# Optimization experiments

Measured on AMD Instinct MI355X. Metric: run time of the kernel, lower is better.

Reference implementation:

```python
import jax, jax.numpy as jnp
import numpy as np

B, L, C, H = 4, 2048, 768, 12
D = C // H
MAX_SCALE_MUL = float(np.log(100.0))
BLOCK = 128  # block size for the VAR-style block-causal mask


def _block_causal_bias(L, block):
    # 0 where key-block <= query-block, -inf elsewhere (block lower-triangular)
    bid = np.arange(L) // block
    vis = bid[:, None] >= bid[None, :]
    bias = np.where(vis, 0.0, -np.inf).astype(np.float32)
    return jnp.asarray(bias)[None, None]  # (1,1,L,L)


def setup_inputs() -> dict:
    key = jax.random.key(0)
    ks = jax.random.split(key, 5)
    x = jax.random.normal(ks[0], (B, L, C), dtype=jnp.float32)
    W_qkv = jax.random.normal(ks[1], (3 * C, C), dtype=jnp.float32) * (1.0 / np.sqrt(C))
    q_bias = jnp.zeros((C,), jnp.float32)
    v_bias = jnp.zeros((C,), jnp.float32)
    # module inits scale_mul to log(4.0)
    log_scale_mul = jnp.full((1, H, 1, 1), np.log(4.0), jnp.float32)
    W_proj = jax.random.normal(ks[2], (C, C), dtype=jnp.float32) * (1.0 / np.sqrt(C))
    b_proj = jnp.zeros((C,), jnp.float32)
    attn_bias = _block_causal_bias(L, BLOCK)
    return {"x": x, "attn_bias": attn_bias, "W_qkv": W_qkv, "q_bias": q_bias,
            "v_bias": v_bias, "log_scale_mul": log_scale_mul,
            "W_proj": W_proj, "b_proj": b_proj}


def _l2norm(t, eps=1e-12):
    n = jnp.linalg.norm(t, axis=-1, keepdims=True)
    return t / jnp.maximum(n, eps)


def reference(x, attn_bias, W_qkv, q_bias, v_bias, log_scale_mul, W_proj, b_proj):
    Bx, Lx, Cx = x.shape
    # qkv projection with concatenated (q_bias, zero_k_bias, v_bias)
    bias = jnp.concatenate([q_bias, jnp.zeros_like(q_bias), v_bias])
    qkv = x @ W_qkv.T + bias                      # (B,L,3C)
    qkv = qkv.reshape(Bx, Lx, 3, H, D)
    q, k, v = jnp.moveaxis(qkv, 2, 0)             # each (B,L,H,D)
    q = jnp.swapaxes(q, 1, 2)                     # (B,H,L,D)
    k = jnp.swapaxes(k, 1, 2)
    v = jnp.swapaxes(v, 1, 2)
    # cos-attention: L2-normalize q,k; head-wise learnable scale on q; scale=1
    scale_mul = jnp.exp(jnp.minimum(log_scale_mul, MAX_SCALE_MUL))  # (1,H,1,1)
    q = _l2norm(q) * scale_mul
    k = _l2norm(k)
    scores = jnp.einsum('bhld,bhmd->bhlm', q, k) + attn_bias
    attn = jax.nn.softmax(scores, axis=-1)
    o = jnp.einsum('bhlm,bhmd->bhld', attn, v)    # (B,H,L,D)
    o = jnp.swapaxes(o, 1, 2).reshape(Bx, Lx, Cx)
    return o @ W_proj.T + b_proj
```

## Files before the change

### kernel.cpp

```cpp
#include <hip/hip_runtime.h>
#include <hip/hip_bf16.h>

#define DEV __device__ __forceinline__

typedef __bf16 bf16x8 __attribute__((ext_vector_type(8)));
typedef float  f32x4  __attribute__((ext_vector_type(4)));

typedef __attribute__((address_space(3))) unsigned int LDSU;
typedef __attribute__((address_space(1))) const unsigned int GLBU;

DEV unsigned short f2b(float f){
  __bf16 h = (__bf16)f;
  return __builtin_bit_cast(unsigned short, h);
}

static constexpr float MAXLOG = 4.60517018598809136804f;
static constexpr float L2E    = 1.44269504088896340736f;

DEV ushort4 cvt4(float4 v){
  ushort4 o; o.x = f2b(v.x); o.y = f2b(v.y); o.z = f2b(v.z); o.w = f2b(v.w); return o;
}
__global__ void cvt3_kernel(const float4* __restrict__ a, ushort4* __restrict__ da, int na,
                            const float4* __restrict__ b, ushort4* __restrict__ db, int nb,
                            const float4* __restrict__ c, ushort4* __restrict__ dc, int nc){
  int i = blockIdx.x * 256 + threadIdx.x;
  if (i < na) { da[i] = cvt4(a[i]); return; }
  i -= na;
  if (i < nb) { db[i] = cvt4(b[i]); return; }
  i -= nb;
  if (i < nc) { dc[i] = cvt4(c[i]); }
}

__global__ __launch_bounds__(512) void qkv_gemm(
    const unsigned short* __restrict__ X,
    const unsigned short* __restrict__ W,
    const float* __restrict__ qbias, const float* __restrict__ vbias,
    const float* __restrict__ lsm,
    unsigned short* __restrict__ Qo, unsigned short* __restrict__ Ko,
    unsigned short* __restrict__ Vo)
{
  __shared__ char smem[65536];
  const int tid = threadIdx.x;
  const int l = tid & 63, w = tid >> 6;
  const int wr = w >> 1, wc = w & 1;
  const int lr = l & 15, lg = l >> 4;
  const int tm = blockIdx.x % 64;
  const int tn = blockIdx.x / 64;
  const int m0 = tm * 128, n0 = tn * 128;

  f32x4 acc[2][4];
  #pragma unroll
  for (int i=0;i<2;i++)
    #pragma unroll
    for (int j=0;j<4;j++) acc[i][j] = (f32x4){0.f,0.f,0.f,0.f};

  #pragma unroll
  for (int c=0;c<2;++c){
    int chunk = c*512 + tid;
    int row = chunk >> 3;
    int scc = (chunk & 7) ^ (row & 7);
    __builtin_amdgcn_global_load_lds((GLBU*)(X + (size_t)(m0+row)*768 + scc*8),
                                     (LDSU*)(smem + chunk*16), 16, 0, 0);
    __builtin_amdgcn_global_load_lds((GLBU*)(W + (size_t)(n0+row)*768 + scc*8),
                                     (LDSU*)(smem + 32768 + chunk*16), 16, 0, 0);
  }

  for (int kt = 0; kt < 12; ++kt){
    __syncthreads();
    const int pc = kt & 1;
    char* Acur = smem + pc*16384;
    char* Bcur = smem + 32768 + pc*16384;

    if (kt + 1 < 12){
      const int k1 = (kt+1)*64;
      char* Anxt = smem + (pc^1)*16384;
      char* Bnxt = smem + 32768 + (pc^1)*16384;
      #pragma unroll
      for (int c=0;c<2;++c){
        int chunk = c*512 + tid;
        int row = chunk >> 3;
        int scc = (chunk & 7) ^ (row & 7);
        __builtin_amdgcn_global_load_lds((GLBU*)(X + (size_t)(m0+row)*768 + k1 + scc*8),
                                         (LDSU*)(Anxt + chunk*16), 16, 0, 0);
        __builtin_amdgcn_global_load_lds((GLBU*)(W + (size_t)(n0+row)*768 + k1 + scc*8),
                                         (LDSU*)(Bnxt + chunk*16), 16, 0, 0);
      }
    }

    #pragma unroll
    for (int kk = 0; kk < 2; ++kk){
      bf16x8 af[2], bfv[4];
      #pragma unroll
      for (int m=0;m<2;m++){
        int row = wr*32 + m*16 + lr;
        int byte = kk*64 + lg*16;
        af[m] = *(const bf16x8*)(Acur + row*128 + (byte ^ ((row&7)<<4)));
      }
      #pragma unroll
      for (int n=0;n<4;n++){
        int row = wc*64 + n*16 + lr;
        int byte = kk*64 + lg*16;
        bfv[n] = *(const bf16x8*)(Bcur + row*128 + (byte ^ ((row&7)<<4)));
      }
      #pragma unroll
      for (int m=0;m<2;m++)
        #pragma unroll
        for (int n=0;n<4;n++)
          acc[m][n] = __builtin_amdgcn_mfma_f32_16x16x32_bf16(af[m], bfv[n], acc[m][n], 0, 0, 0);
    }
  }

  const int nb = n0 + wc*64;
  const int seg = nb / 768;
  const int h = (nb % 768) / 64;
  float mul = 1.0f;
  if (seg == 0) mul = __expf(fminf(lsm[h], MAXLOG)) * L2E;
  float bias_v[4];
  #pragma unroll
  for (int n=0;n<4;n++){
    int d = n*16 + lr;
    bias_v[n] = (seg==0) ? qbias[h*64+d] : (seg==2 ? vbias[h*64+d] : 0.f);
  }
  unsigned short* dst = (seg==0) ? Qo : (seg==1 ? Ko : Vo);
  #pragma unroll
  for (int m=0;m<2;m++){
    #pragma unroll
    for (int r=0;r<4;r++){
      float vals[4]; float ss = 0.f;
      #pragma unroll
      for (int n=0;n<4;n++){ float v = acc[m][n][r] + bias_v[n]; vals[n] = v; ss += v*v; }
      ss += __shfl_xor(ss,1); ss += __shfl_xor(ss,2);
      ss += __shfl_xor(ss,4); ss += __shfl_xor(ss,8);
      float sc = (seg==2) ? 1.f : mul / fmaxf(sqrtf(ss), 1e-12f);
      int grow = m0 + wr*32 + m*16 + lg*4 + r;
      int b = grow >> 11, lrow = grow & 2047;
      size_t base = (((size_t)(b*12 + h))*2048 + lrow)*64;
      #pragma unroll
      for (int n=0;n<4;n++) dst[base + n*16 + lr] = f2b(vals[n]*sc);
    }
  }
}

__global__ __launch_bounds__(512) void attn_kernel(
    const unsigned short* __restrict__ Q,
    const unsigned short* __restrict__ K,
    const unsigned short* __restrict__ V,
    const float* __restrict__ lsm,
    unsigned short* __restrict__ O)
{
  __shared__ char smem[49152];
  const int tid = threadIdx.x;
  const int l = tid & 63, w = tid >> 6;
  char* Plds = smem + 32768 + w*2048;
  const int lr = l & 15, lg = l >> 4;

  const int bid = blockIdx.x;
  const int qb = 15 - (bid / 48);
  const int bh = bid % 48;
  const int h = bh % 12;
  const size_t plane = (size_t)bh * (2048*64);
  const int q0 = qb*128 + w*16;

  const float M = __expf(fminf(lsm[h], MAXLOG)) * L2E;

  bf16x8 qf[2];
  #pragma unroll
  for (int ki=0;ki<2;ki++)
    qf[ki] = *(const bf16x8*)(Q + plane + (size_t)(q0 + lr)*64 + ki*32 + lg*8);

  float lsum = 0.f;
  f32x4 of[4];
  #pragma unroll
  for (int di=0;di<4;di++) of[di] = (f32x4){0.f,0.f,0.f,0.f};

  const int krow = tid >> 3;
  const int kscc = (tid & 7) ^ (krow & 7);
  const int rv  = tid & 63;
  const int c0v = (tid >> 6) * 8;

  const int nt = (qb + 1) * 2;

  {
    const unsigned short* Kt0 = K + plane;
    const unsigned short* Vt0 = V + plane;
    __builtin_amdgcn_global_load_lds((GLBU*)(Kt0 + krow*64 + kscc*8),
                                     (LDSU*)(smem + tid*16), 16, 0, 0);
    bf16x8 a = *(const bf16x8*)(Vt0 + rv*64 + c0v);
    #pragma unroll
    for (int j=0;j<8;j++)
      *(__bf16*)(smem + 16384 + (c0v+j)*128 + ((2*rv) ^ (j<<4))) = a[j];
  }

  for (int t = 0; t < nt; ++t){
    __syncthreads();
    const int pc = t & 1;
    char* Kcur = smem + pc*8192;
    char* Vcur = smem + 16384 + pc*8192;
    char* Knxt = smem + (pc^1)*8192;
    char* Vnxt = smem + 16384 + (pc^1)*8192;
    const bool pre = (t+1) < nt;

    bf16x8 nv;
    if (pre){
      const unsigned short* Kt1 = K + plane + (size_t)(t+1)*4096;
      const unsigned short* Vt1 = V + plane + (size_t)(t+1)*4096;
      __builtin_amdgcn_global_load_lds((GLBU*)(Kt1 + krow*64 + kscc*8),
                                       (LDSU*)(Knxt + tid*16), 16, 0, 0);
      nv = *(const bf16x8*)(Vt1 + rv*64 + c0v);
    }

    f32x4 s[4];
    #pragma unroll
    for (int ni=0;ni<4;ni++) s[ni] = (f32x4){0.f,0.f,0.f,0.f};
    #pragma unroll
    for (int ki=0;ki<2;ki++){
      bf16x8 kb[4];
      #pragma unroll
      for (int ni=0;ni<4;ni++){
        int key = ni*16 + lr;
        int byte = ki*64 + lg*16;
        kb[ni] = *(const bf16x8*)(Kcur + key*128 + (byte ^ ((key&7)<<4)));
      }
      __builtin_amdgcn_s_setprio(1);
      #pragma unroll
      for (int ni=0;ni<4;ni++)
        s[ni] = __builtin_amdgcn_mfma_f32_16x16x32_bf16(kb[ni], qf[ki], s[ni], 0, 0, 0);
      __builtin_amdgcn_s_setprio(0);
    }

    {
      const int row = lr;
      float a16 = 0.f;
      #pragma unroll
      for (int ni=0;ni<4;ni++){
        float p0 = __builtin_amdgcn_exp2f(s[ni][0] - M);
        float p1 = __builtin_amdgcn_exp2f(s[ni][1] - M);
        float p2 = __builtin_amdgcn_exp2f(s[ni][2] - M);
        float p3 = __builtin_amdgcn_exp2f(s[ni][3] - M);
        a16 += (p0 + p1) + (p2 + p3);
        uint2 uv;
        uv.x = (unsigned)f2b(p0) | ((unsigned)f2b(p1) << 16);
        uv.y = (unsigned)f2b(p2) | ((unsigned)f2b(p3) << 16);
        *(uint2*)(Plds + row*128 + ((ni*32 + lg*8) ^ ((row&7)<<4))) = uv;
      }
      lsum += a16;
    }
    asm volatile("s_waitcnt lgkmcnt(0)" ::: "memory");
    __builtin_amdgcn_sched_barrier(0);

    #pragma unroll
    for (int ki=0;ki<2;ki++){
      bf16x8 pa, vbf[4];
      {
        int row = lr;
        int byte = ki*64 + lg*16;
        pa = *(const bf16x8*)(Plds + row*128 + (byte ^ ((row&7)<<4)));
      }
      #pragma unroll
      for (int di=0;di<4;di++){
        int d = di*16 + lr;
        int byte = ki*64 + lg*16;
        vbf[di] = *(const bf16x8*)(Vcur + d*128 + (byte ^ ((d&7)<<4)));
      }
      __builtin_amdgcn_s_setprio(1);
      #pragma unroll
      for (int di=0;di<4;di++)
        of[di] = __builtin_amdgcn_mfma_f32_16x16x32_bf16(pa, vbf[di], of[di], 0, 0, 0);
      __builtin_amdgcn_s_setprio(0);
    }

    if (pre){
      #pragma unroll
      for (int j=0;j<8;j++)
        *(__bf16*)(Vnxt + (c0v+j)*128 + ((2*rv) ^ (j<<4))) = nv[j];
    }
  }

  {
    float sum = lsum;
    sum += __shfl_xor(sum,16); sum += __shfl_xor(sum,32);
    lsum = sum;
  }
  const int b = bh / 12;
  #pragma unroll
  for (int r=0;r<4;r++){
    float inv = 1.f / __shfl(lsum, lg*4 + r);
    int row = q0 + lg*4 + r;
    size_t base = ((size_t)(b*2048) + row)*768 + h*64;
    #pragma unroll
    for (int di=0;di<4;di++)
      O[base + di*16 + lr] = f2b(of[di][r]*inv);
  }
}

__global__ __launch_bounds__(256) void proj_gemm(
    const unsigned short* __restrict__ A,
    const unsigned short* __restrict__ W,
    const float* __restrict__ bias,
    float* __restrict__ out)
{
  __shared__ char smem[16384];
  char* Alds = smem;
  char* Blds = smem + 8192;

  const int tid = threadIdx.x;
  const int l = tid & 63, w = tid >> 6;
  const int lr = l & 15, lg = l >> 4;
  const int tm = blockIdx.x % 128;
  const int tn = blockIdx.x / 128;
  const int m0 = tm * 64, n0 = tn * 64;

  f32x4 acc[4];
  #pragma unroll
  for (int j=0;j<4;j++) acc[j] = (f32x4){0.f,0.f,0.f,0.f};

  for (int kt = 0; kt < 12; ++kt){
    const int k0 = kt * 64;
    __syncthreads();
    #pragma unroll
    for (int c = 0; c < 2; ++c){
      int chunk = c*256 + tid;
      int row = chunk >> 3;
      int scc = (chunk & 7) ^ (row & 7);
      __builtin_amdgcn_global_load_lds((GLBU*)(A + (size_t)(m0+row)*768 + k0 + scc*8),
                                       (LDSU*)(Alds + (c*256 + w*64)*16), 16, 0, 0);
      __builtin_amdgcn_global_load_lds((GLBU*)(W + (size_t)(n0+row)*768 + k0 + scc*8),
                                       (LDSU*)(Blds + (c*256 + w*64)*16), 16, 0, 0);
    }
    __syncthreads();
    #pragma unroll
    for (int kk = 0; kk < 2; ++kk){
      bf16x8 af, bfv[4];
      {
        int row = w*16 + lr;
        int byte = kk*64 + lg*16;
        af = *(const bf16x8*)(Alds + row*128 + (byte ^ ((row&7)<<4)));
      }
      #pragma unroll
      for (int n=0;n<4;n++){
        int row = n*16 + lr;
        int byte = kk*64 + lg*16;
        bfv[n] = *(const bf16x8*)(Blds + row*128 + (byte ^ ((row&7)<<4)));
      }
      #pragma unroll
      for (int n=0;n<4;n++)
        acc[n] = __builtin_amdgcn_mfma_f32_16x16x32_bf16(af, bfv[n], acc[n], 0, 0, 0);
    }
  }

  #pragma unroll
  for (int r=0;r<4;r++){
    int grow = m0 + w*16 + lg*4 + r;
    #pragma unroll
    for (int n=0;n<4;n++){
      int colg = n0 + n*16 + lr;
      out[(size_t)grow*768 + colg] = acc[n][r] + bias[colg];
    }
  }
}

extern "C" void kernel_launch(void* const* d_in, const int* in_sizes, int n_in,
                              void* d_out, int out_size, void* d_ws, size_t ws_size,
                              hipStream_t stream)
{
  const float* x     = (const float*)d_in[0];
  const float* Wqkv  = (const float*)d_in[2];
  const float* qbias = (const float*)d_in[3];
  const float* vbias = (const float*)d_in[4];
  const float* lsm   = (const float*)d_in[5];
  const float* Wproj = (const float*)d_in[6];
  const float* bproj = (const float*)d_in[7];
  float* out = (float*)d_out;

  char* ws = (char*)d_ws;
  size_t off = 0;
  auto alloc = [&](size_t bytes)->char*{
    char* p = ws + off; off += (bytes + 255) & ~(size_t)255; return p;
  };
  unsigned short* xb  = (unsigned short*)alloc((size_t)8192*768*2);
  unsigned short* wqb = (unsigned short*)alloc((size_t)2304*768*2);
  unsigned short* wpb = (unsigned short*)alloc((size_t)768*768*2);
  unsigned short* qn  = (unsigned short*)alloc((size_t)48*2048*64*2);
  unsigned short* kn  = (unsigned short*)alloc((size_t)48*2048*64*2);
  unsigned short* vn  = (unsigned short*)alloc((size_t)48*2048*64*2);
  unsigned short* ob  = (unsigned short*)alloc((size_t)8192*768*2);

  cvt3_kernel<<<8448, 256, 0, stream>>>((const float4*)x,     (ushort4*)xb,  1572864,
                                        (const float4*)Wqkv,  (ushort4*)wqb,  442368,
                                        (const float4*)Wproj, (ushort4*)wpb,  147456);
  qkv_gemm<<<64*18, 512, 0, stream>>>(xb, wqb, qbias, vbias, lsm, qn, kn, vn);
  attn_kernel<<<768, 512, 0, stream>>>(qn, kn, vn, lsm, ob);
  proj_gemm<<<128*12, 256, 0, stream>>>(ob, wpb, bproj, out);
}
```

Baseline: 119.6 us.

## Double attention query tile per block to reuse K/V tiles across 256 queries

Each attention block now handles 256 query rows (32 per wave) instead of 128, so every K/V tile staged in LDS feeds twice as many MFMAs, and the grid is halved to 384 blocks. Waves in the lower half of the block skip the final key tiles that fall outside their causal range but still take part in the loads and barriers. This cuts repeated K/V global traffic and loop overhead at the cost of more LDS (64KB), more registers, fewer blocks for the 256 CUs, and some idle waves in the last tiles.

```diff
diff --git a/kernel.cpp b/kernel.cpp
--- a/kernel.cpp
+++ b/kernel.cpp
@@ -148,37 +148,42 @@
     const float* __restrict__ lsm,
     unsigned short* __restrict__ O)
 {
-  __shared__ char smem[49152];
+  __shared__ char smem[65536];
   const int tid = threadIdx.x;
   const int l = tid & 63, w = tid >> 6;
-  char* Plds = smem + 32768 + w*2048;
+  char* Plds = smem + 32768 + w*4096;
   const int lr = l & 15, lg = l >> 4;
 
   const int bid = blockIdx.x;
-  const int qb = 15 - (bid / 48);
+  const int pb = 7 - (bid / 48);
   const int bh = bid % 48;
   const int h = bh % 12;
   const size_t plane = (size_t)bh * (2048*64);
-  const int q0 = qb*128 + w*16;
+  const int q0 = pb*256 + w*32;
+
+  const int my_nt  = (2*pb + 1 + (w >> 2)) * 2;
+  const int nt_max = (2*pb + 2) * 2;
 
   const float M = __expf(fminf(lsm[h], MAXLOG)) * L2E;
 
-  bf16x8 qf[2];
-  #pragma unroll
-  for (int ki=0;ki<2;ki++)
-    qf[ki] = *(const bf16x8*)(Q + plane + (size_t)(q0 + lr)*64 + ki*32 + lg*8);
-
-  float lsum = 0.f;
-  f32x4 of[4];
-  #pragma unroll
-  for (int di=0;di<4;di++) of[di] = (f32x4){0.f,0.f,0.f,0.f};
+  bf16x8 qf[2][2];
+  #pragma unroll
+  for (int mi=0;mi<2;mi++)
+    #pragma unroll
+    for (int ki=0;ki<2;ki++)
+      qf[mi][ki] = *(const bf16x8*)(Q + plane + (size_t)(q0 + mi*16 + lr)*64 + ki*32 + lg*8);
+
+  float lsum[2] = {0.f, 0.f};
+  f32x4 of[2][4];
+  #pragma unroll
+  for (int mi=0;mi<2;mi++)
+    #pragma unroll
+    for (int di=0;di<4;di++) of[mi][di] = (f32x4){0.f,0.f,0.f,0.f};
 
   const int krow = tid >> 3;
   const int kscc = (tid & 7) ^ (krow & 7);
   const int rv  = tid & 63;
   const int c0v = (tid >> 6) * 8;
-
-  const int nt = (qb + 1) * 2;
 
   {
     const unsigned short* Kt0 = K + plane;
@@ -191,14 +196,14 @@
       *(__bf16*)(smem + 16384 + (c0v+j)*128 + ((2*rv) ^ (j<<4))) = a[j];
   }
 
-  for (int t = 0; t < nt; ++t){
+  for (int t = 0; t < nt_max; ++t){
     __syncthreads();
     const int pc = t & 1;
     char* Kcur = smem + pc*8192;
     char* Vcur = smem + 16384 + pc*8192;
     char* Knxt = smem + (pc^1)*8192;
     char* Vnxt = smem + 16384 + (pc^1)*8192;
-    const bool pre = (t+1) < nt;
+    const bool pre = (t+1) < nt_max;
 
     bf16x8 nv;
     if (pre){
@@ -209,64 +214,74 @@
       nv = *(const bf16x8*)(Vt1 + rv*64 + c0v);
     }
 
-    f32x4 s[4];
-    #pragma unroll
-    for (int ni=0;ni<4;ni++) s[ni] = (f32x4){0.f,0.f,0.f,0.f};
-    #pragma unroll
-    for (int ki=0;ki<2;ki++){
-      bf16x8 kb[4];
-      #pragma unroll
-      for (int ni=0;ni<4;ni++){
-        int key = ni*16 + lr;
-        int byte = ki*64 + lg*16;
-        kb[ni] = *(const bf16x8*)(Kcur + key*128 + (byte ^ ((key&7)<<4)));
-      }
-      __builtin_amdgcn_s_setprio(1);
-      #pragma unroll
-      for (int ni=0;ni<4;ni++)
-        s[ni] = __builtin_amdgcn_mfma_f32_16x16x32_bf16(kb[ni], qf[ki], s[ni], 0, 0, 0);
-      __builtin_amdgcn_s_setprio(0);
-    }
-
-    {
-      const int row = lr;
-      float a16 = 0.f;
-      #pragma unroll
-      for (int ni=0;ni<4;ni++){
-        float p0 = __builtin_amdgcn_exp2f(s[ni][0] - M);
-        float p1 = __builtin_amdgcn_exp2f(s[ni][1] - M);
-        float p2 = __builtin_amdgcn_exp2f(s[ni][2] - M);
-        float p3 = __builtin_amdgcn_exp2f(s[ni][3] - M);
-        a16 += (p0 + p1) + (p2 + p3);
-        uint2 uv;
-        uv.x = (unsigned)f2b(p0) | ((unsigned)f2b(p1) << 16);
-        uv.y = (unsigned)f2b(p2) | ((unsigned)f2b(p3) << 16);
-        *(uint2*)(Plds + row*128 + ((ni*32 + lg*8) ^ ((row&7)<<4))) = uv;
-      }
-      lsum += a16;
-    }
-    asm volatile("s_waitcnt lgkmcnt(0)" ::: "memory");
-    __builtin_amdgcn_sched_barrier(0);
-
-    #pragma unroll
-    for (int ki=0;ki<2;ki++){
-      bf16x8 pa, vbf[4];
-      {
-        int row = lr;
-        int byte = ki*64 + lg*16;
-        pa = *(const bf16x8*)(Plds + row*128 + (byte ^ ((row&7)<<4)));
-      }
-      #pragma unroll
-      for (int di=0;di<4;di++){
-        int d = di*16 + lr;
-        int byte = ki*64 + lg*16;
-        vbf[di] = *(const bf16x8*)(Vcur + d*128 + (byte ^ ((d&7)<<4)));
-      }
-      __builtin_amdgcn_s_setprio(1);
-      #pragma unroll
-      for (int di=0;di<4;di++)
-        of[di] = __builtin_amdgcn_mfma_f32_16x16x32_bf16(pa, vbf[di], of[di], 0, 0, 0);
-      __builtin_amdgcn_s_setprio(0);
+    if (t < my_nt){
+      f32x4 s[2][4];
+      #pragma unroll
+      for (int mi=0;mi<2;mi++)
+        #pragma unroll
+        for (int ni=0;ni<4;ni++) s[mi][ni] = (f32x4){0.f,0.f,0.f,0.f};
+      #pragma unroll
+      for (int ki=0;ki<2;ki++){
+        bf16x8 kb[4];
+        #pragma unroll
+        for (int ni=0;ni<4;ni++){
+          int key = ni*16 + lr;
+          int byte = ki*64 + lg*16;
+          kb[ni] = *(const bf16x8*)(Kcur + key*128 + (byte ^ ((key&7)<<4)));
+        }
+        __builtin_amdgcn_s_setprio(1);
+        #pragma unroll
+        for (int mi=0;mi<2;mi++)
+          #pragma unroll
+          for (int ni=0;ni<4;ni++)
+            s[mi][ni] = __builtin_amdgcn_mfma_f32_16x16x32_bf16(kb[ni], qf[mi][ki], s[mi][ni], 0, 0, 0);
+        __builtin_amdgcn_s_setprio(0);
+      }
+
+      #pragma unroll
+      for (int mi=0;mi<2;mi++){
+        const int row = mi*16 + lr;
+        float a16 = 0.f;
+        #pragma unroll
+        for (int ni=0;ni<4;ni++){
+          float p0 = __builtin_amdgcn_exp2f(s[mi][ni][0] - M);
+          float p1 = __builtin_amdgcn_exp2f(s[mi][ni][1] - M);
+          float p2 = __builtin_amdgcn_exp2f(s[mi][ni][2] - M);
+          float p3 = __builtin_amdgcn_exp2f(s[mi][ni][3] - M);
+          a16 += (p0 + p1) + (p2 + p3);
+          uint2 uv;
+          uv.x = (unsigned)f2b(p0) | ((unsigned)f2b(p1) << 16);
+          uv.y = (unsigned)f2b(p2) | ((unsigned)f2b(p3) << 16);
+          *(uint2*)(Plds + row*128 + ((ni*32 + lg*8) ^ ((row&7)<<4))) = uv;
+        }
+        lsum[mi] += a16;
+      }
+      asm volatile("s_waitcnt lgkmcnt(0)" ::: "memory");
+      __builtin_amdgcn_sched_barrier(0);
+
+      #pragma unroll
+      for (int ki=0;ki<2;ki++){
+        bf16x8 pa[2], vbf[4];
+        #pragma unroll
+        for (int mi=0;mi<2;mi++){
+          int row = mi*16 + lr;
+          int byte = ki*64 + lg*16;
+          pa[mi] = *(const bf16x8*)(Plds + row*128 + (byte ^ ((row&7)<<4)));
+        }
+        #pragma unroll
+        for (int di=0;di<4;di++){
+          int d = di*16 + lr;
+          int byte = ki*64 + lg*16;
+          vbf[di] = *(const bf16x8*)(Vcur + d*128 + (byte ^ ((d&7)<<4)));
+        }
+        __builtin_amdgcn_s_setprio(1);
+        #pragma unroll
+        for (int mi=0;mi<2;mi++)
+          #pragma unroll
+          for (int di=0;di<4;di++)
+            of[mi][di] = __builtin_amdgcn_mfma_f32_16x16x32_bf16(pa[mi], vbf[di], of[mi][di], 0, 0, 0);
+        __builtin_amdgcn_s_setprio(0);
+      }
     }
 
     if (pre){
@@ -276,20 +291,24 @@
     }
   }
 
-  {
-    float sum = lsum;
+  #pragma unroll
+  for (int mi=0;mi<2;mi++){
+    float sum = lsum[mi];
     sum += __shfl_xor(sum,16); sum += __shfl_xor(sum,32);
-    lsum = sum;
+    lsum[mi] = sum;
   }
   const int b = bh / 12;
   #pragma unroll
-  for (int r=0;r<4;r++){
-    float inv = 1.f / __shfl(lsum, lg*4 + r);
-    int row = q0 + lg*4 + r;
-    size_t base = ((size_t)(b*2048) + row)*768 + h*64;
-    #pragma unroll
-    for (int di=0;di<4;di++)
-      O[base + di*16 + lr] = f2b(of[di][r]*inv);
+  for (int mi=0;mi<2;mi++){
+    #pragma unroll
+    for (int r=0;r<4;r++){
+      float inv = 1.f / __shfl(lsum[mi], lg*4 + r);
+      int row = q0 + mi*16 + lg*4 + r;
+      size_t base = ((size_t)(b*2048) + row)*768 + h*64;
+      #pragma unroll
+      for (int di=0;di<4;di++)
+        O[base + di*16 + lr] = f2b(of[mi][di][r]*inv);
+    }
   }
 }
 
@@ -389,6 +408,6 @@
                                         (const float4*)Wqkv,  (ushort4*)wqb,  442368,
                                         (const float4*)Wproj, (ushort4*)wpb,  147456);
   qkv_gemm<<<64*18, 512, 0, stream>>>(xb, wqb, qbias, vbias, lsm, qn, kn, vn);
-  attn_kernel<<<768, 512, 0, stream>>>(qn, kn, vn, lsm, ob);
+  attn_kernel<<<384, 512, 0, stream>>>(qn, kn, vn, lsm, ob);
   proj_gemm<<<128*12, 256, 0, stream>>>(ob, wpb, bproj, out);
 }
```

Result: slower. 134.2 us (+12.2%).
